# Kernel optimization log

Measured on AMD Instinct MI355X. Metric: run time of the kernel, lower is better.

Reference implementation:

```python
import jax, jax.numpy as jnp
import numpy as np

K_SIZE = 5
N_HEAD = 4


def flow_to_grid(flow, k_size=K_SIZE):
    # flow: (n, 2, h, w) -> normalized sample coords vx, vy: (n, k^2, h, w)
    n, _, h, w = flow.shape
    pad = (k_size - 1) // 2
    gy, gx = jnp.meshgrid(jnp.arange(h, dtype=flow.dtype),
                          jnp.arange(w, dtype=flow.dtype), indexing='ij')
    shift = jnp.arange(k_size, dtype=flow.dtype) - pad
    sy, sx = jnp.meshgrid(shift, shift, indexing='ij')  # (k,k), 'ij' like torch
    sy = sy.reshape(-1, 1, 1)  # (k^2,1,1)
    sx = sx.reshape(-1, 1, 1)
    sample_x = gx[None] + sx  # (k^2,h,w)
    sample_y = gy[None] + sy
    vx = sample_x[None] + flow[:, 0][:, None]  # (n,k^2,h,w)
    vy = sample_y[None] + flow[:, 1][:, None]
    vx = 2.0 * vx / max(w - 1, 1) - 1.0
    vy = 2.0 * vy / max(h - 1, 1) - 1.0
    return vx, vy


def grid_sample_zeros(feat, gx, gy):
    # feat: (C,H,W); gx, gy: (K2,h,w) normalized in [-1,1]
    # bilinear, padding_mode='zeros', align_corners=True
    C, H, W = feat.shape
    x = (gx + 1.0) * 0.5 * (W - 1)
    y = (gy + 1.0) * 0.5 * (H - 1)
    x0 = jnp.floor(x)
    y0 = jnp.floor(y)
    wx = x - x0
    wy = y - y0

    def gather(xi, yi):
        inb = (xi >= 0) & (xi <= W - 1) & (yi >= 0) & (yi <= H - 1)
        xi_c = jnp.clip(xi, 0, W - 1).astype(jnp.int32)
        yi_c = jnp.clip(yi, 0, H - 1).astype(jnp.int32)
        val = feat[:, yi_c, xi_c]  # (C,K2,h,w)
        return val * inb.astype(feat.dtype)

    v00 = gather(x0, y0)
    v01 = gather(x0 + 1, y0)
    v10 = gather(x0, y0 + 1)
    v11 = gather(x0 + 1, y0 + 1)
    return (v00 * (1 - wx) * (1 - wy) + v01 * wx * (1 - wy)
            + v10 * (1 - wx) * wy + v11 * wx * wy)  # (C,K2,h,w)


def setup_inputs() -> dict:
    key = jax.random.key(0)
    ks = jax.random.split(key, 8)
    n, c, h, w = 4, 128, 64, 64
    scale = 1.0 / np.sqrt(c)
    return {
        'q': jax.random.normal(ks[0], (n, c, h, w), jnp.float32),
        'k': jax.random.normal(ks[1], (n, c, h, w), jnp.float32),
        'v': jax.random.normal(ks[2], (n, c, h, w), jnp.float32),
        'flow': jax.random.normal(ks[3], (n, 2, h, w), jnp.float32) * 4.0,
        'Wq': jax.random.normal(ks[4], (c, c), jnp.float32) * scale,
        'Wk': jax.random.normal(ks[5], (c, c), jnp.float32) * scale,
        'Wv': jax.random.normal(ks[6], (c, c), jnp.float32) * scale,
        'Wfc': jax.random.normal(ks[7], (c, c), jnp.float32) * scale,
    }


def reference(q, k, v, flow, Wq, Wk, Wv, Wfc):
    # 1x1 convs == channel matmuls
    qp = jnp.einsum('oc,nchw->nohw', Wq, q)
    kp = jnp.einsum('oc,nchw->nohw', Wk, k)
    vp = jnp.einsum('oc,nchw->nohw', Wv, v)

    vx, vy = flow_to_grid(flow, K_SIZE)  # (n,K2,h,w) each
    ksamp = jax.vmap(grid_sample_zeros)(kp, vx, vy)  # (n,C,K2,h,w)
    vsamp = jax.vmap(grid_sample_zeros)(vp, vx, vy)

    n, C, K2, h, w = ksamp.shape
    d = C // N_HEAD
    qh = qp.reshape(n, N_HEAD, d, h, w)
    kh = ksamp.reshape(n, N_HEAD, d, K2, h, w)
    vh = vsamp.reshape(n, N_HEAD, d, K2, h, w)

    logits = jnp.einsum('nhdyx,nhdkyx->nhkyx', qh / jnp.sqrt(jnp.float32(d)), kh)
    attn = jax.nn.softmax(logits, axis=2)  # softmax over the k^2 window
    out = jnp.einsum('nhkyx,nhdkyx->nhdyx', attn, vh)
    out = out.reshape(n, N_HEAD * d, h, w)
    out = jnp.einsum('oc,nchw->nohw', Wfc, out)
    return out, attn
```

## Files before the change

### kernel.cpp

```cpp
#include <hip/hip_runtime.h>

constexpr int NB = 4;
constexpr int CC = 128;
constexpr int HH = 64;
constexpr int WW = 64;
constexpr int HWp = HH * WW;
constexpr int NHEADS = 4;
constexpr int K2 = 25;

typedef unsigned int   uint32;
typedef unsigned short ushort16;
typedef __attribute__((ext_vector_type(8))) short bf16x8;
typedef __attribute__((ext_vector_type(4))) float f32x4;

__device__ __forceinline__ ushort16 f2bf(float x) {
    uint32 b = __float_as_uint(x);
    return (ushort16)((b + 0x7FFFu + ((b >> 16) & 1u)) >> 16);
}
__device__ __forceinline__ uint32 pack2(float lo, float hi) {
    return ((uint32)f2bf(hi) << 16) | (uint32)f2bf(lo);
}
__device__ __forceinline__ float bf_lo(uint32 u) { return __uint_as_float(u << 16); }
__device__ __forceinline__ float bf_hi(uint32 u) { return __uint_as_float(u & 0xFFFF0000u); }

__global__ __launch_bounds__(256) void wconv_kernel(
    const float* __restrict__ Wq, const float* __restrict__ Wk,
    const float* __restrict__ Wv, const float* __restrict__ Wfc,
    ushort16* __restrict__ wbf)
{
    int i = blockIdx.x * 256 + threadIdx.x;
    int m = i >> 12;
    int j = i & 4095;
    const float* s = (m == 0) ? Wq : ((m == 1) ? Wk : ((m == 2) ? Wv : Wfc));
    float4 f = reinterpret_cast<const float4*>(s)[j];
    uint32 w0 = pack2(f.x, f.y);
    uint32 w1 = pack2(f.z, f.w);
    uint32* d = reinterpret_cast<uint32*>(wbf + (size_t)m * 16384);
    d[j * 2]     = w0;
    d[j * 2 + 1] = w1;
}

__global__ __launch_bounds__(256) void proj_mfma(
    const float* __restrict__ q, const float* __restrict__ k, const float* __restrict__ v,
    const ushort16* __restrict__ wbf,
    ushort16* __restrict__ qp, ushort16* __restrict__ kp, ushort16* __restrict__ vp)
{
    __shared__ __align__(16) ushort16 lx[64 * 132];

    int blk = blockIdx.x;
    int p   = blk >> 8;
    int rem = blk & 255;
    int n   = rem >> 6;
    int pt  = rem & 63;
    int pix0 = pt * 64;

    const float*    X  = (p == 0) ? q  : ((p == 1) ? k  : v);
    ushort16*       O  = (p == 0) ? qp : ((p == 1) ? kp : vp);
    const ushort16* Wb = wbf + (size_t)p * 16384;
    const float*    Xb = X + (size_t)n * CC * HWp + pix0;

    int lane = threadIdx.x & 63;
    int cg   = threadIdx.x >> 6;

#pragma unroll
    for (int i = 0; i < 16; ++i) {
        int c0 = i * 8 + cg * 2;
        float a = Xb[c0 * HWp + lane];
        float b = Xb[(c0 + 1) * HWp + lane];
        *reinterpret_cast<uint32*>(&lx[lane * 132 + c0]) = pack2(a, b);
    }
    __syncthreads();

    int wid = threadIdx.x >> 6;
    int wr  = wid >> 1, wc = wid & 1;
    int p16 = lane & 15, kg = lane >> 4;

    f32x4 acc[4][2] = {};

#pragma unroll
    for (int k0 = 0; k0 < 128; k0 += 32) {
        bf16x8 A[4], B[2];
#pragma unroll
        for (int ai = 0; ai < 4; ++ai) {
            int o = wr * 64 + ai * 16 + p16;
            A[ai] = *reinterpret_cast<const bf16x8*>(&Wb[o * 128 + k0 + kg * 8]);
        }
#pragma unroll
        for (int bj = 0; bj < 2; ++bj) {
            int px = wc * 32 + bj * 16 + p16;
            const ushort16* sp = &lx[px * 132 + k0 + kg * 8];
            struct { unsigned long long lo, hi; } t;
            t.lo = *reinterpret_cast<const unsigned long long*>(sp);
            t.hi = *reinterpret_cast<const unsigned long long*>(sp + 4);
            B[bj] = __builtin_bit_cast(bf16x8, t);
        }
#pragma unroll
        for (int ai = 0; ai < 4; ++ai)
#pragma unroll
            for (int bj = 0; bj < 2; ++bj)
                acc[ai][bj] = __builtin_amdgcn_mfma_f32_16x16x32_bf16(
                    A[ai], B[bj], acc[ai][bj], 0, 0, 0);
    }

    ushort16* Ob = O + (size_t)(n * HWp + pix0) * CC;
#pragma unroll
    for (int ai = 0; ai < 4; ++ai) {
        int ob = wr * 64 + ai * 16 + kg * 4;
#pragma unroll
        for (int bj = 0; bj < 2; ++bj) {
            int px = wc * 32 + bj * 16 + p16;
            uint32* dst = reinterpret_cast<uint32*>(&Ob[(size_t)px * CC + ob]);
            dst[0] = pack2(acc[ai][bj][0], acc[ai][bj][1]);
            dst[1] = pack2(acc[ai][bj][2], acc[ai][bj][3]);
        }
    }
}


#define KVLOAD(BUF, BASE, R) { \
    const ushort16* r_ = (BASE) + roff[R]; \
    _Pragma("unroll") \
    for (int rx = 0; rx < 6; ++rx) \
        BUF[rx] = *reinterpret_cast<const uint4*>(r_ + coff[rx]); }

#define DOT8(U) \
    fmaf(qv[7], bf_hi((U).w), fmaf(qv[6], bf_lo((U).w), \
    fmaf(qv[5], bf_hi((U).z), fmaf(qv[4], bf_lo((U).z), \
    fmaf(qv[3], bf_hi((U).y), fmaf(qv[2], bf_lo((U).y), \
    fmaf(qv[1], bf_hi((U).x), qv[0] * bf_lo((U).x))))))))

#define KCONSUME(BUF, R) { \
    float pd_[6]; \
    _Pragma("unroll") \
    for (int rx = 0; rx < 6; ++rx) pd_[rx] = DOT8(BUF[rx]); \
    float hbr_[5]; \
    _Pragma("unroll") \
    for (int kx = 0; kx < 5; ++kx) \
        hbr_[kx] = pd_[kx] * XA[kx] + pd_[kx + 1] * XB[kx + 1]; \
    if ((R) < 5) { \
        _Pragma("unroll") \
        for (int kx = 0; kx < 5; ++kx) l[(R) * 5 + kx] = hbr_[kx] * YT[R]; } \
    if ((R) >= 1) { \
        _Pragma("unroll") \
        for (int kx = 0; kx < 5; ++kx) \
            l[((R) - 1) * 5 + kx] = fmaf(hbr_[kx], YB[R], l[((R) - 1) * 5 + kx]); } }

#define VCONSUME(BUF, R) { \
    float lhc_[6]; \
    if ((R) < 5) { \
        lhc_[0] = l[(R) * 5 + 0] * XA[0]; \
        _Pragma("unroll") \
        for (int rx = 1; rx < 5; ++rx) \
            lhc_[rx] = l[(R) * 5 + rx] * XA[rx] + l[(R) * 5 + rx - 1] * XB[rx]; \
        lhc_[5] = l[(R) * 5 + 4] * XB[5]; \
    } else { \
        _Pragma("unroll") \
        for (int rx = 0; rx < 6; ++rx) lhc_[rx] = 0.f; \
    } \
    _Pragma("unroll") \
    for (int rx = 0; rx < 6; ++rx) { \
        float w6_ = lhc_[rx] * YT[R] + lhp[rx] * YB[R]; \
        uint4 u_ = BUF[rx]; \
        acc[0] = fmaf(bf_lo(u_.x), w6_, acc[0]); \
        acc[1] = fmaf(bf_hi(u_.x), w6_, acc[1]); \
        acc[2] = fmaf(bf_lo(u_.y), w6_, acc[2]); \
        acc[3] = fmaf(bf_hi(u_.y), w6_, acc[3]); \
        acc[4] = fmaf(bf_lo(u_.z), w6_, acc[4]); \
        acc[5] = fmaf(bf_hi(u_.z), w6_, acc[5]); \
        acc[6] = fmaf(bf_lo(u_.w), w6_, acc[6]); \
        acc[7] = fmaf(bf_hi(u_.w), w6_, acc[7]); \
    } \
    _Pragma("unroll") \
    for (int rx = 0; rx < 6; ++rx) lhp[rx] = lhc_[rx]; }

__global__ __launch_bounds__(64) void attn_kernel(
    ushort16* qoh,
    const ushort16* __restrict__ kp, const ushort16* __restrict__ vp,
    const float* __restrict__ flow,
    float* __restrict__ attn)
{
    int blk = blockIdx.x;
    int swz = ((blk & 7) << 9) + (blk >> 3);
    int tid = threadIdx.x;
    int pix = swz * 4 + (tid >> 4);
    int lg  = tid & 15;
    int c0  = lg * 8;
    int n   = pix >> 12;
    int yx  = pix & 4095;
    int y   = yx >> 6, x = yx & 63;

    float fx = flow[((size_t)n * 2 + 0) * HWp + yx];
    float fy = flow[((size_t)n * 2 + 1) * HWp + yx];
    float pxf = (float)x + fx, pyf = (float)y + fy;
    float X0 = floorf(pxf), Y0 = floorf(pyf);
    float wx = pxf - X0,    wy = pyf - Y0;
    int ix0 = (int)X0 - 2,  iy0 = (int)Y0 - 2;

    int coff[6], roff[6];
    float XA[6], XB[6], YT[6], YB[6];
#pragma unroll
    for (int r = 0; r < 6; ++r) {
        int xi = ix0 + r;
        float mx = (xi >= 0 && xi < WW) ? 1.f : 0.f;
        int xc = xi < 0 ? 0 : (xi > WW - 1 ? WW - 1 : xi);
        coff[r] = xc * CC;
        XA[r] = (1.f - wx) * mx;
        XB[r] = wx * mx;
        int yi = iy0 + r;
        float my = (yi >= 0 && yi < HH) ? 1.f : 0.f;
        int yc = yi < 0 ? 0 : (yi > HH - 1 ? HH - 1 : yi);
        roff[r] = yc * (WW * CC);
        YT[r] = (1.f - wy) * my;
        YB[r] = wy * my;
    }

    const ushort16* kb  = kp + (size_t)n * HWp * CC + c0;
    const ushort16* vbp = vp + (size_t)n * HWp * CC + c0;
    ushort16* qb = qoh + (size_t)pix * CC + c0;

    uint4 qraw = *reinterpret_cast<const uint4*>(qb);
    float qv[8] = { bf_lo(qraw.x), bf_hi(qraw.x), bf_lo(qraw.y), bf_hi(qraw.y),
                    bf_lo(qraw.z), bf_hi(qraw.z), bf_lo(qraw.w), bf_hi(qraw.w) };

    float l[25];
    {
        uint4 kA[6], kB[6];
        KVLOAD(kA, kb, 0)
        KVLOAD(kB, kb, 1)
        KCONSUME(kA, 0)
        KVLOAD(kA, kb, 2)
        KCONSUME(kB, 1)
        KVLOAD(kB, kb, 3)
        KCONSUME(kA, 2)
        KVLOAD(kA, kb, 4)
        KCONSUME(kB, 3)
        KVLOAD(kB, kb, 5)
        KCONSUME(kA, 4)
        KCONSUME(kB, 5)
    }

    uint4 vA[6], vB[6];
    KVLOAD(vA, vbp, 0)
    KVLOAD(vB, vbp, 1)

#pragma unroll
    for (int kk = 0; kk < 25; ++kk) {
        float s = l[kk];
        s += __shfl_xor(s, 1);
        s += __shfl_xor(s, 2);
        l[kk] = s * 0.17677669529663687f;
    }

    float m = l[0];
#pragma unroll
    for (int kk = 1; kk < 25; ++kk) m = fmaxf(m, l[kk]);
    float sum = 0.f;
#pragma unroll
    for (int kk = 0; kk < 25; ++kk) { l[kk] = __expf(l[kk] - m); sum += l[kk]; }
    float inv = 1.f / sum;
#pragma unroll
    for (int kk = 0; kk < 25; ++kk) l[kk] *= inv;

    float acc[8] = {0.f, 0.f, 0.f, 0.f, 0.f, 0.f, 0.f, 0.f};
    float lhp[6] = {0.f, 0.f, 0.f, 0.f, 0.f, 0.f};
    VCONSUME(vA, 0)
    KVLOAD(vA, vbp, 2)
    VCONSUME(vB, 1)
    KVLOAD(vB, vbp, 3)
    VCONSUME(vA, 2)
    KVLOAD(vA, vbp, 4)
    VCONSUME(vB, 3)
    KVLOAD(vB, vbp, 5)
    VCONSUME(vA, 4)
    VCONSUME(vB, 5)

    {
        int head = lg >> 2, j = lg & 3;
        float* ab = attn + (((size_t)n * NHEADS + head) * K2) * HWp + yx;
#pragma unroll
        for (int kk = 0; kk < 25; ++kk)
            if ((kk & 3) == j) ab[(size_t)kk * HWp] = l[kk];
    }

    uint4 o;
    o.x = pack2(acc[0], acc[1]);
    o.y = pack2(acc[2], acc[3]);
    o.z = pack2(acc[4], acc[5]);
    o.w = pack2(acc[6], acc[7]);
    *reinterpret_cast<uint4*>(qb) = o;
}

__global__ __launch_bounds__(256) void fc_mfma(
    const ushort16* __restrict__ oh, const ushort16* __restrict__ wfcb,
    float* __restrict__ out)
{
    int blk = blockIdx.x;
    int gp0 = blk * 64;
    int n   = gp0 >> 12;
    int yx0 = gp0 & 4095;

    int lane = threadIdx.x & 63;
    int wid  = threadIdx.x >> 6;
    int wr = wid >> 1, wc = wid & 1;
    int p16 = lane & 15, kg = lane >> 4;

    const ushort16* ohb = oh + (size_t)gp0 * CC;

    f32x4 acc[4][2] = {};

#pragma unroll
    for (int k0 = 0; k0 < 128; k0 += 32) {
        bf16x8 A[4], B[2];
#pragma unroll
        for (int ai = 0; ai < 4; ++ai) {
            int o = wr * 64 + ai * 16 + p16;
            A[ai] = *reinterpret_cast<const bf16x8*>(&wfcb[o * 128 + k0 + kg * 8]);
        }
#pragma unroll
        for (int bj = 0; bj < 2; ++bj) {
            int px = wc * 32 + bj * 16 + p16;
            B[bj] = *reinterpret_cast<const bf16x8*>(&ohb[(size_t)px * CC + k0 + kg * 8]);
        }
#pragma unroll
        for (int ai = 0; ai < 4; ++ai)
#pragma unroll
            for (int bj = 0; bj < 2; ++bj)
                acc[ai][bj] = __builtin_amdgcn_mfma_f32_16x16x32_bf16(
                    A[ai], B[bj], acc[ai][bj], 0, 0, 0);
    }

    float* ob = out + (size_t)n * CC * HWp + yx0;
#pragma unroll
    for (int ai = 0; ai < 4; ++ai) {
        int o = wr * 64 + ai * 16 + kg * 4;
#pragma unroll
        for (int bj = 0; bj < 2; ++bj) {
            int px = wc * 32 + bj * 16 + p16;
#pragma unroll
            for (int r = 0; r < 4; ++r)
                ob[(size_t)(o + r) * HWp + px] = acc[ai][bj][r];
        }
    }
}

extern "C" void kernel_launch(void* const* d_in, const int* in_sizes, int n_in,
                              void* d_out, int out_size, void* d_ws, size_t ws_size,
                              hipStream_t stream)
{
    const float* q    = (const float*)d_in[0];
    const float* k    = (const float*)d_in[1];
    const float* v    = (const float*)d_in[2];
    const float* flow = (const float*)d_in[3];
    const float* Wq   = (const float*)d_in[4];
    const float* Wk   = (const float*)d_in[5];
    const float* Wv   = (const float*)d_in[6];
    const float* Wfc  = (const float*)d_in[7];

    float* out  = (float*)d_out;
    float* attn = out + (size_t)NB * CC * HWp;

    ushort16* ws = (ushort16*)d_ws;
    size_t slab = (size_t)NB * HWp * CC;
    ushort16* qp  = ws;
    ushort16* kp  = ws + slab;
    ushort16* vp  = ws + 2 * slab;
    ushort16* wbf = ws + 3 * slab;

    wconv_kernel<<<dim3(64), dim3(256), 0, stream>>>(Wq, Wk, Wv, Wfc, wbf);
    proj_mfma<<<dim3(768), dim3(256), 0, stream>>>(q, k, v, wbf, qp, kp, vp);
    attn_kernel<<<dim3(4096), dim3(64), 0, stream>>>(qp, kp, vp, flow, attn);
    fc_mfma<<<dim3(256), dim3(256), 0, stream>>>(qp, wbf + 3 * 16384, out);
}
```

Baseline: 50.45 us.

## Map one pixel per wave with two channels per lane in attention kernel

The attention kernel now gives each 64-lane wave a single pixel, with each lane handling 2 channels via 32-bit loads, where before 16 lanes each handled 8 channels per pixel. The grid grows to 16384 blocks and the head-sum reduction gains two more shuffle stages. This cuts register pressure and raises parallelism (launch bounds now ask for 4 blocks). In exchange, loads are narrower per lane, there are more shuffles, and per-thread flow and weight setup is repeated across four times as many threads.

```diff
diff --git a/kernel.cpp b/kernel.cpp
--- a/kernel.cpp
+++ b/kernel.cpp
@@ -117,22 +117,17 @@
 }
 
 
-#define KVLOAD(BUF, BASE, R) { \
+#define KVLOAD1(BUF, BASE, R) { \
     const ushort16* r_ = (BASE) + roff[R]; \
     _Pragma("unroll") \
     for (int rx = 0; rx < 6; ++rx) \
-        BUF[rx] = *reinterpret_cast<const uint4*>(r_ + coff[rx]); }
-
-#define DOT8(U) \
-    fmaf(qv[7], bf_hi((U).w), fmaf(qv[6], bf_lo((U).w), \
-    fmaf(qv[5], bf_hi((U).z), fmaf(qv[4], bf_lo((U).z), \
-    fmaf(qv[3], bf_hi((U).y), fmaf(qv[2], bf_lo((U).y), \
-    fmaf(qv[1], bf_hi((U).x), qv[0] * bf_lo((U).x))))))))
-
-#define KCONSUME(BUF, R) { \
+        BUF[rx] = *reinterpret_cast<const uint32*>(r_ + coff[rx]); }
+
+#define KCONSUME1(BUF, R) { \
     float pd_[6]; \
     _Pragma("unroll") \
-    for (int rx = 0; rx < 6; ++rx) pd_[rx] = DOT8(BUF[rx]); \
+    for (int rx = 0; rx < 6; ++rx) \
+        pd_[rx] = fmaf(q1, bf_hi(BUF[rx]), q0 * bf_lo(BUF[rx])); \
     float hbr_[5]; \
     _Pragma("unroll") \
     for (int kx = 0; kx < 5; ++kx) \
@@ -145,7 +140,7 @@
         for (int kx = 0; kx < 5; ++kx) \
             l[((R) - 1) * 5 + kx] = fmaf(hbr_[kx], YB[R], l[((R) - 1) * 5 + kx]); } }
 
-#define VCONSUME(BUF, R) { \
+#define VCONSUME1(BUF, R) { \
     float lhc_[6]; \
     if ((R) < 5) { \
         lhc_[0] = l[(R) * 5 + 0] * XA[0]; \
@@ -160,31 +155,23 @@
     _Pragma("unroll") \
     for (int rx = 0; rx < 6; ++rx) { \
         float w6_ = lhc_[rx] * YT[R] + lhp[rx] * YB[R]; \
-        uint4 u_ = BUF[rx]; \
-        acc[0] = fmaf(bf_lo(u_.x), w6_, acc[0]); \
-        acc[1] = fmaf(bf_hi(u_.x), w6_, acc[1]); \
-        acc[2] = fmaf(bf_lo(u_.y), w6_, acc[2]); \
-        acc[3] = fmaf(bf_hi(u_.y), w6_, acc[3]); \
-        acc[4] = fmaf(bf_lo(u_.z), w6_, acc[4]); \
-        acc[5] = fmaf(bf_hi(u_.z), w6_, acc[5]); \
-        acc[6] = fmaf(bf_lo(u_.w), w6_, acc[6]); \
-        acc[7] = fmaf(bf_hi(u_.w), w6_, acc[7]); \
+        uint32 u_ = BUF[rx]; \
+        acc0 = fmaf(bf_lo(u_), w6_, acc0); \
+        acc1 = fmaf(bf_hi(u_), w6_, acc1); \
     } \
     _Pragma("unroll") \
     for (int rx = 0; rx < 6; ++rx) lhp[rx] = lhc_[rx]; }
 
-__global__ __launch_bounds__(64) void attn_kernel(
+__global__ __launch_bounds__(64, 4) void attn_kernel(
     ushort16* qoh,
     const ushort16* __restrict__ kp, const ushort16* __restrict__ vp,
     const float* __restrict__ flow,
     float* __restrict__ attn)
 {
     int blk = blockIdx.x;
-    int swz = ((blk & 7) << 9) + (blk >> 3);
-    int tid = threadIdx.x;
-    int pix = swz * 4 + (tid >> 4);
-    int lg  = tid & 15;
-    int c0  = lg * 8;
+    int pix = ((blk & 7) << 11) + (blk >> 3);
+    int lane = threadIdx.x;
+    int c0  = lane * 2;
     int n   = pix >> 12;
     int yx  = pix & 4095;
     int y   = yx >> 6, x = yx & 63;
@@ -218,36 +205,37 @@
     const ushort16* vbp = vp + (size_t)n * HWp * CC + c0;
     ushort16* qb = qoh + (size_t)pix * CC + c0;
 
-    uint4 qraw = *reinterpret_cast<const uint4*>(qb);
-    float qv[8] = { bf_lo(qraw.x), bf_hi(qraw.x), bf_lo(qraw.y), bf_hi(qraw.y),
-                    bf_lo(qraw.z), bf_hi(qraw.z), bf_lo(qraw.w), bf_hi(qraw.w) };
+    uint32 qpk = *reinterpret_cast<const uint32*>(qb);
+    float q0 = bf_lo(qpk), q1 = bf_hi(qpk);
 
     float l[25];
     {
-        uint4 kA[6], kB[6];
-        KVLOAD(kA, kb, 0)
-        KVLOAD(kB, kb, 1)
-        KCONSUME(kA, 0)
-        KVLOAD(kA, kb, 2)
-        KCONSUME(kB, 1)
-        KVLOAD(kB, kb, 3)
-        KCONSUME(kA, 2)
-        KVLOAD(kA, kb, 4)
-        KCONSUME(kB, 3)
-        KVLOAD(kB, kb, 5)
-        KCONSUME(kA, 4)
-        KCONSUME(kB, 5)
-    }
-
-    uint4 vA[6], vB[6];
-    KVLOAD(vA, vbp, 0)
-    KVLOAD(vB, vbp, 1)
+        uint32 kA[6], kB[6];
+        KVLOAD1(kA, kb, 0)
+        KVLOAD1(kB, kb, 1)
+        KCONSUME1(kA, 0)
+        KVLOAD1(kA, kb, 2)
+        KCONSUME1(kB, 1)
+        KVLOAD1(kB, kb, 3)
+        KCONSUME1(kA, 2)
+        KVLOAD1(kA, kb, 4)
+        KCONSUME1(kB, 3)
+        KVLOAD1(kB, kb, 5)
+        KCONSUME1(kA, 4)
+        KCONSUME1(kB, 5)
+    }
+
+    uint32 vA[6], vB[6];
+    KVLOAD1(vA, vbp, 0)
+    KVLOAD1(vB, vbp, 1)
 
 #pragma unroll
     for (int kk = 0; kk < 25; ++kk) {
         float s = l[kk];
         s += __shfl_xor(s, 1);
         s += __shfl_xor(s, 2);
+        s += __shfl_xor(s, 4);
+        s += __shfl_xor(s, 8);
         l[kk] = s * 0.17677669529663687f;
     }
 
@@ -261,33 +249,28 @@
 #pragma unroll
     for (int kk = 0; kk < 25; ++kk) l[kk] *= inv;
 
-    float acc[8] = {0.f, 0.f, 0.f, 0.f, 0.f, 0.f, 0.f, 0.f};
+    float acc0 = 0.f, acc1 = 0.f;
     float lhp[6] = {0.f, 0.f, 0.f, 0.f, 0.f, 0.f};
-    VCONSUME(vA, 0)
-    KVLOAD(vA, vbp, 2)
-    VCONSUME(vB, 1)
-    KVLOAD(vB, vbp, 3)
-    VCONSUME(vA, 2)
-    KVLOAD(vA, vbp, 4)
-    VCONSUME(vB, 3)
-    KVLOAD(vB, vbp, 5)
-    VCONSUME(vA, 4)
-    VCONSUME(vB, 5)
+    VCONSUME1(vA, 0)
+    KVLOAD1(vA, vbp, 2)
+    VCONSUME1(vB, 1)
+    KVLOAD1(vB, vbp, 3)
+    VCONSUME1(vA, 2)
+    KVLOAD1(vA, vbp, 4)
+    VCONSUME1(vB, 3)
+    KVLOAD1(vB, vbp, 5)
+    VCONSUME1(vA, 4)
+    VCONSUME1(vB, 5)
 
     {
-        int head = lg >> 2, j = lg & 3;
+        int head = lane >> 4, lih = lane & 15;
         float* ab = attn + (((size_t)n * NHEADS + head) * K2) * HWp + yx;
 #pragma unroll
         for (int kk = 0; kk < 25; ++kk)
-            if ((kk & 3) == j) ab[(size_t)kk * HWp] = l[kk];
-    }
-
-    uint4 o;
-    o.x = pack2(acc[0], acc[1]);
-    o.y = pack2(acc[2], acc[3]);
-    o.z = pack2(acc[4], acc[5]);
-    o.w = pack2(acc[6], acc[7]);
-    *reinterpret_cast<uint4*>(qb) = o;
+            if ((kk & 15) == lih) ab[(size_t)kk * HWp] = l[kk];
+    }
+
+    *reinterpret_cast<uint32*>(qb) = pack2(acc0, acc1);
 }
 
 __global__ __launch_bounds__(256) void fc_mfma(
@@ -368,6 +351,6 @@
 
     wconv_kernel<<<dim3(64), dim3(256), 0, stream>>>(Wq, Wk, Wv, Wfc, wbf);
     proj_mfma<<<dim3(768), dim3(256), 0, stream>>>(q, k, v, wbf, qp, kp, vp);
-    attn_kernel<<<dim3(4096), dim3(64), 0, stream>>>(qp, kp, vp, flow, attn);
+    attn_kernel<<<dim3(16384), dim3(64), 0, stream>>>(qp, kp, vp, flow, attn);
     fc_mfma<<<dim3(256), dim3(256), 0, stream>>>(qp, wbf + 3 * 16384, out);
 }
```

New measurement: 77.96 us. 1.55x slower.

## Stream K/V gathers through LDS with async global_load_lds four-deep pipeline

Applied to the files above, without the earlier changes.

Replaces the register double-buffered K/V gathers in the attention kernel with global_load_lds direct-to-LDS loads across four slots. Waits are handled manually with vmcnt/lgkmcnt and sched barriers so up to four rows of 6 loads each stay in flight. The goal is to hide gather latency and cut register pressure. In exchange it adds 24KB of LDS per 64-thread block, which may limit occupancy, and it depends on the hand-counted waitcnt values being correct.

```diff
diff --git a/kernel.cpp b/kernel.cpp
--- a/kernel.cpp
+++ b/kernel.cpp
@@ -117,11 +117,19 @@
 }
 
 
-#define KVLOAD(BUF, BASE, R) { \
-    const ushort16* r_ = (BASE) + roff[R]; \
-    _Pragma("unroll") \
-    for (int rx = 0; rx < 6; ++rx) \
-        BUF[rx] = *reinterpret_cast<const uint4*>(r_ + coff[rx]); }
+#define WAITVM(N) { asm volatile("s_waitcnt vmcnt(" #N ")" ::: "memory"); \
+                    __builtin_amdgcn_sched_barrier(0); }
+#define LGKM0     { asm volatile("s_waitcnt lgkmcnt(0)" ::: "memory"); \
+                    __builtin_amdgcn_sched_barrier(0); }
+
+#define ISSUE(BASE, R, SLOT) { \
+    const ushort16* rb_ = (BASE) + roff[R]; \
+    _Pragma("unroll") \
+    for (int rx = 0; rx < 6; ++rx) { \
+        __builtin_amdgcn_global_load_lds( \
+            (const __attribute__((address_space(1))) void*)(rb_ + coff[rx]), \
+            (__attribute__((address_space(3))) void*)&lds[(SLOT) * 6144 + rx * 1024], \
+            16, 0, 0); } }
 
 #define DOT8(U) \
     fmaf(qv[7], bf_hi((U).w), fmaf(qv[6], bf_lo((U).w), \
@@ -129,10 +137,14 @@
     fmaf(qv[3], bf_hi((U).y), fmaf(qv[2], bf_lo((U).y), \
     fmaf(qv[1], bf_hi((U).x), qv[0] * bf_lo((U).x))))))))
 
-#define KCONSUME(BUF, R) { \
+#define KC(SLOT, R) { \
     float pd_[6]; \
     _Pragma("unroll") \
-    for (int rx = 0; rx < 6; ++rx) pd_[rx] = DOT8(BUF[rx]); \
+    for (int rx = 0; rx < 6; ++rx) { \
+        uint4 u_ = *reinterpret_cast<const uint4*>( \
+            &lds[(SLOT) * 6144 + rx * 1024 + tid * 16]); \
+        pd_[rx] = DOT8(u_); \
+    } \
     float hbr_[5]; \
     _Pragma("unroll") \
     for (int kx = 0; kx < 5; ++kx) \
@@ -145,7 +157,7 @@
         for (int kx = 0; kx < 5; ++kx) \
             l[((R) - 1) * 5 + kx] = fmaf(hbr_[kx], YB[R], l[((R) - 1) * 5 + kx]); } }
 
-#define VCONSUME(BUF, R) { \
+#define VC(SLOT, R) { \
     float lhc_[6]; \
     if ((R) < 5) { \
         lhc_[0] = l[(R) * 5 + 0] * XA[0]; \
@@ -160,7 +172,8 @@
     _Pragma("unroll") \
     for (int rx = 0; rx < 6; ++rx) { \
         float w6_ = lhc_[rx] * YT[R] + lhp[rx] * YB[R]; \
-        uint4 u_ = BUF[rx]; \
+        uint4 u_ = *reinterpret_cast<const uint4*>( \
+            &lds[(SLOT) * 6144 + rx * 1024 + tid * 16]); \
         acc[0] = fmaf(bf_lo(u_.x), w6_, acc[0]); \
         acc[1] = fmaf(bf_hi(u_.x), w6_, acc[1]); \
         acc[2] = fmaf(bf_lo(u_.y), w6_, acc[2]); \
@@ -179,6 +192,8 @@
     const float* __restrict__ flow,
     float* __restrict__ attn)
 {
+    __shared__ __align__(16) unsigned char lds[4 * 6144];
+
     int blk = blockIdx.x;
     int swz = ((blk & 7) << 9) + (blk >> 3);
     int tid = threadIdx.x;
@@ -222,26 +237,20 @@
     float qv[8] = { bf_lo(qraw.x), bf_hi(qraw.x), bf_lo(qraw.y), bf_hi(qraw.y),
                     bf_lo(qraw.z), bf_hi(qraw.z), bf_lo(qraw.w), bf_hi(qraw.w) };
 
+    WAITVM(0);
+
+    ISSUE(kb, 0, 0)
+    ISSUE(kb, 1, 1)
+    ISSUE(kb, 2, 2)
+    ISSUE(kb, 3, 3)
+
     float l[25];
-    {
-        uint4 kA[6], kB[6];
-        KVLOAD(kA, kb, 0)
-        KVLOAD(kB, kb, 1)
-        KCONSUME(kA, 0)
-        KVLOAD(kA, kb, 2)
-        KCONSUME(kB, 1)
-        KVLOAD(kB, kb, 3)
-        KCONSUME(kA, 2)
-        KVLOAD(kA, kb, 4)
-        KCONSUME(kB, 3)
-        KVLOAD(kB, kb, 5)
-        KCONSUME(kA, 4)
-        KCONSUME(kB, 5)
-    }
-
-    uint4 vA[6], vB[6];
-    KVLOAD(vA, vbp, 0)
-    KVLOAD(vB, vbp, 1)
+    WAITVM(18);  KC(0, 0)  LGKM0;  ISSUE(kb, 4, 0)
+    WAITVM(18);  KC(1, 1)  LGKM0;  ISSUE(kb, 5, 1)
+    WAITVM(18);  KC(2, 2)  LGKM0;  ISSUE(vbp, 0, 2)
+    WAITVM(18);  KC(3, 3)  LGKM0;  ISSUE(vbp, 1, 3)
+    WAITVM(18);  KC(0, 4)  LGKM0;  ISSUE(vbp, 2, 0)
+    WAITVM(18);  KC(1, 5)  LGKM0;  ISSUE(vbp, 3, 1)
 
 #pragma unroll
     for (int kk = 0; kk < 25; ++kk) {
@@ -263,16 +272,12 @@
 
     float acc[8] = {0.f, 0.f, 0.f, 0.f, 0.f, 0.f, 0.f, 0.f};
     float lhp[6] = {0.f, 0.f, 0.f, 0.f, 0.f, 0.f};
-    VCONSUME(vA, 0)
-    KVLOAD(vA, vbp, 2)
-    VCONSUME(vB, 1)
-    KVLOAD(vB, vbp, 3)
-    VCONSUME(vA, 2)
-    KVLOAD(vA, vbp, 4)
-    VCONSUME(vB, 3)
-    KVLOAD(vB, vbp, 5)
-    VCONSUME(vA, 4)
-    VCONSUME(vB, 5)
+    WAITVM(18);  VC(2, 0)  LGKM0;  ISSUE(vbp, 4, 2)
+    WAITVM(18);  VC(3, 1)  LGKM0;  ISSUE(vbp, 5, 3)
+    WAITVM(12);  VC(0, 2)
+    WAITVM(6);   VC(1, 3)
+    WAITVM(0);   VC(2, 4)
+                 VC(3, 5)
 
     {
         int head = lg >> 2, j = lg & 3;
```

After: 59.00 us. 16.9% more time.

## Split attention sample columns across two half-waves per pixel

Applied to the files above, without the earlier changes.

The attention kernel now gives each pixel 32 lanes instead of 16. Lanes in the two halves each load and dot three of the six sample columns, then swap partial dot products with shuffles and sum the V accumulators at the end. The grid doubles to 8192 blocks. This halves the per-thread gather loads and registers to raise parallelism and memory-level concurrency. The cost is extra shuffles, duplicated softmax work, and half the lanes idling on the attn and output writes.

```diff
diff --git a/kernel.cpp b/kernel.cpp
--- a/kernel.cpp
+++ b/kernel.cpp
@@ -117,11 +117,11 @@
 }
 
 
-#define KVLOAD(BUF, BASE, R) { \
+#define KVLOAD2(BUF, BASE, R) { \
     const ushort16* r_ = (BASE) + roff[R]; \
     _Pragma("unroll") \
-    for (int rx = 0; rx < 6; ++rx) \
-        BUF[rx] = *reinterpret_cast<const uint4*>(r_ + coff[rx]); }
+    for (int kq = 0; kq < 3; ++kq) \
+        BUF[kq] = *reinterpret_cast<const uint4*>(r_ + coffL[kq]); }
 
 #define DOT8(U) \
     fmaf(qv[7], bf_hi((U).w), fmaf(qv[6], bf_lo((U).w), \
@@ -129,10 +129,18 @@
     fmaf(qv[3], bf_hi((U).y), fmaf(qv[2], bf_lo((U).y), \
     fmaf(qv[1], bf_hi((U).x), qv[0] * bf_lo((U).x))))))))
 
-#define KCONSUME(BUF, R) { \
+#define KC2(BUF, R) { \
+    float do_[3], ds_[3]; \
+    _Pragma("unroll") \
+    for (int kq = 0; kq < 3; ++kq) do_[kq] = DOT8(BUF[kq]); \
+    _Pragma("unroll") \
+    for (int kq = 0; kq < 3; ++kq) ds_[kq] = __shfl_xor(do_[kq], 16); \
     float pd_[6]; \
     _Pragma("unroll") \
-    for (int rx = 0; rx < 6; ++rx) pd_[rx] = DOT8(BUF[rx]); \
+    for (int kq = 0; kq < 3; ++kq) { \
+        pd_[2 * kq]     = hsel ? ds_[kq] : do_[kq]; \
+        pd_[2 * kq + 1] = hsel ? do_[kq] : ds_[kq]; \
+    } \
     float hbr_[5]; \
     _Pragma("unroll") \
     for (int kx = 0; kx < 5; ++kx) \
@@ -145,7 +153,7 @@
         for (int kx = 0; kx < 5; ++kx) \
             l[((R) - 1) * 5 + kx] = fmaf(hbr_[kx], YB[R], l[((R) - 1) * 5 + kx]); } }
 
-#define VCONSUME(BUF, R) { \
+#define VC2(BUF, R) { \
     float lhc_[6]; \
     if ((R) < 5) { \
         lhc_[0] = l[(R) * 5 + 0] * XA[0]; \
@@ -158,9 +166,11 @@
         for (int rx = 0; rx < 6; ++rx) lhc_[rx] = 0.f; \
     } \
     _Pragma("unroll") \
-    for (int rx = 0; rx < 6; ++rx) { \
-        float w6_ = lhc_[rx] * YT[R] + lhp[rx] * YB[R]; \
-        uint4 u_ = BUF[rx]; \
+    for (int kq = 0; kq < 3; ++kq) { \
+        float lc_ = hsel ? lhc_[2 * kq + 1] : lhc_[2 * kq]; \
+        float lp_ = hsel ? lhp[2 * kq + 1] : lhp[2 * kq]; \
+        float w6_ = lc_ * YT[R] + lp_ * YB[R]; \
+        uint4 u_ = BUF[kq]; \
         acc[0] = fmaf(bf_lo(u_.x), w6_, acc[0]); \
         acc[1] = fmaf(bf_hi(u_.x), w6_, acc[1]); \
         acc[2] = fmaf(bf_lo(u_.y), w6_, acc[2]); \
@@ -180,14 +190,16 @@
     float* __restrict__ attn)
 {
     int blk = blockIdx.x;
-    int swz = ((blk & 7) << 9) + (blk >> 3);
-    int tid = threadIdx.x;
-    int pix = swz * 4 + (tid >> 4);
-    int lg  = tid & 15;
-    int c0  = lg * 8;
-    int n   = pix >> 12;
-    int yx  = pix & 4095;
-    int y   = yx >> 6, x = yx & 63;
+    int swz = ((blk & 7) << 10) + (blk >> 3);
+    int lane = threadIdx.x;
+    int px   = lane >> 5;
+    bool hsel = (lane & 16) != 0;
+    int h    = hsel ? 1 : 0;
+    int c    = lane & 15;
+    int pix  = swz * 2 + px;
+    int n    = pix >> 12;
+    int yx   = pix & 4095;
+    int y    = yx >> 6, x = yx & 63;
 
     float fx = flow[((size_t)n * 2 + 0) * HWp + yx];
     float fy = flow[((size_t)n * 2 + 1) * HWp + yx];
@@ -196,14 +208,12 @@
     float wx = pxf - X0,    wy = pyf - Y0;
     int ix0 = (int)X0 - 2,  iy0 = (int)Y0 - 2;
 
-    int coff[6], roff[6];
+    int roff[6];
     float XA[6], XB[6], YT[6], YB[6];
 #pragma unroll
     for (int r = 0; r < 6; ++r) {
         int xi = ix0 + r;
         float mx = (xi >= 0 && xi < WW) ? 1.f : 0.f;
-        int xc = xi < 0 ? 0 : (xi > WW - 1 ? WW - 1 : xi);
-        coff[r] = xc * CC;
         XA[r] = (1.f - wx) * mx;
         XB[r] = wx * mx;
         int yi = iy0 + r;
@@ -213,10 +223,17 @@
         YT[r] = (1.f - wy) * my;
         YB[r] = wy * my;
     }
-
-    const ushort16* kb  = kp + (size_t)n * HWp * CC + c0;
-    const ushort16* vbp = vp + (size_t)n * HWp * CC + c0;
-    ushort16* qb = qoh + (size_t)pix * CC + c0;
+    int coffL[3];
+#pragma unroll
+    for (int kq = 0; kq < 3; ++kq) {
+        int xi = ix0 + 2 * kq + h;
+        int xc = xi < 0 ? 0 : (xi > WW - 1 ? WW - 1 : xi);
+        coffL[kq] = xc * CC + c * 8;
+    }
+
+    const ushort16* kb  = kp + (size_t)n * HWp * CC;
+    const ushort16* vbp = vp + (size_t)n * HWp * CC;
+    ushort16* qb = qoh + (size_t)pix * CC + c * 8;
 
     uint4 qraw = *reinterpret_cast<const uint4*>(qb);
     float qv[8] = { bf_lo(qraw.x), bf_hi(qraw.x), bf_lo(qraw.y), bf_hi(qraw.y),
@@ -224,24 +241,24 @@
 
     float l[25];
     {
-        uint4 kA[6], kB[6];
-        KVLOAD(kA, kb, 0)
-        KVLOAD(kB, kb, 1)
-        KCONSUME(kA, 0)
-        KVLOAD(kA, kb, 2)
-        KCONSUME(kB, 1)
-        KVLOAD(kB, kb, 3)
-        KCONSUME(kA, 2)
-        KVLOAD(kA, kb, 4)
-        KCONSUME(kB, 3)
-        KVLOAD(kB, kb, 5)
-        KCONSUME(kA, 4)
-        KCONSUME(kB, 5)
-    }
-
-    uint4 vA[6], vB[6];
-    KVLOAD(vA, vbp, 0)
-    KVLOAD(vB, vbp, 1)
+        uint4 kA[3], kB[3];
+        KVLOAD2(kA, kb, 0)
+        KVLOAD2(kB, kb, 1)
+        KC2(kA, 0)
+        KVLOAD2(kA, kb, 2)
+        KC2(kB, 1)
+        KVLOAD2(kB, kb, 3)
+        KC2(kA, 2)
+        KVLOAD2(kA, kb, 4)
+        KC2(kB, 3)
+        KVLOAD2(kB, kb, 5)
+        KC2(kA, 4)
+        KC2(kB, 5)
+    }
+
+    uint4 vA[3], vB[3];
+    KVLOAD2(vA, vbp, 0)
+    KVLOAD2(vB, vbp, 1)
 
 #pragma unroll
     for (int kk = 0; kk < 25; ++kk) {
@@ -263,31 +280,36 @@
 
     float acc[8] = {0.f, 0.f, 0.f, 0.f, 0.f, 0.f, 0.f, 0.f};
     float lhp[6] = {0.f, 0.f, 0.f, 0.f, 0.f, 0.f};
-    VCONSUME(vA, 0)
-    KVLOAD(vA, vbp, 2)
-    VCONSUME(vB, 1)
-    KVLOAD(vB, vbp, 3)
-    VCONSUME(vA, 2)
-    KVLOAD(vA, vbp, 4)
-    VCONSUME(vB, 3)
-    KVLOAD(vB, vbp, 5)
-    VCONSUME(vA, 4)
-    VCONSUME(vB, 5)
+    VC2(vA, 0)
+    KVLOAD2(vA, vbp, 2)
+    VC2(vB, 1)
+    KVLOAD2(vB, vbp, 3)
+    VC2(vA, 2)
+    KVLOAD2(vA, vbp, 4)
+    VC2(vB, 3)
+    KVLOAD2(vB, vbp, 5)
+    VC2(vA, 4)
+    VC2(vB, 5)
+
+#pragma unroll
+    for (int i = 0; i < 8; ++i) acc[i] += __shfl_xor(acc[i], 16);
 
     {
-        int head = lg >> 2, j = lg & 3;
+        int head = c >> 2, j = c & 3;
         float* ab = attn + (((size_t)n * NHEADS + head) * K2) * HWp + yx;
 #pragma unroll
         for (int kk = 0; kk < 25; ++kk)
-            if ((kk & 3) == j) ab[(size_t)kk * HWp] = l[kk];
-    }
-
-    uint4 o;
-    o.x = pack2(acc[0], acc[1]);
-    o.y = pack2(acc[2], acc[3]);
-    o.z = pack2(acc[4], acc[5]);
-    o.w = pack2(acc[6], acc[7]);
-    *reinterpret_cast<uint4*>(qb) = o;
+            if (!hsel && (kk & 3) == j) ab[(size_t)kk * HWp] = l[kk];
+    }
+
+    if (!hsel) {
+        uint4 o;
+        o.x = pack2(acc[0], acc[1]);
+        o.y = pack2(acc[2], acc[3]);
+        o.z = pack2(acc[4], acc[5]);
+        o.w = pack2(acc[6], acc[7]);
+        *reinterpret_cast<uint4*>(qb) = o;
+    }
 }
 
 __global__ __launch_bounds__(256) void fc_mfma(
@@ -368,6 +390,6 @@
 
     wconv_kernel<<<dim3(64), dim3(256), 0, stream>>>(Wq, Wk, Wv, Wfc, wbf);
     proj_mfma<<<dim3(768), dim3(256), 0, stream>>>(q, k, v, wbf, qp, kp, vp);
-    attn_kernel<<<dim3(4096), dim3(64), 0, stream>>>(qp, kp, vp, flow, attn);
+    attn_kernel<<<dim3(8192), dim3(64), 0, stream>>>(qp, kp, vp, flow, attn);
     fc_mfma<<<dim3(256), dim3(256), 0, stream>>>(qp, wbf + 3 * 16384, out);
 }
```

Result: slower. 79.14 us (+56.9%).
